# Kernel tuning notes

Hardware: AMD Instinct MI355X
Metric: run time of the kernel (lower is better)

The kernel has to match this reference:

```python
import jax, jax.numpy as jnp
import numpy as np
from jax import lax

DN = ('NCHW', 'OIHW', 'NCHW')

def conv2d(x, w, b, stride):
    y = lax.conv_general_dilated(x, w, (stride, stride), [(1, 1), (1, 1)], dimension_numbers=DN)
    return y + b[None, :, None, None]

def conv_transpose2d(x, w, b):
    # PyTorch ConvTranspose2d(k=3, stride=2, padding=1, output_padding=1)
    # == conv with lhs_dilation=2, pad low = k-1-p = 1, pad high = k-1-p+op = 2,
    # kernel spatially flipped and in/out channel dims swapped.  w: [in, out, kh, kw]
    wf = jnp.flip(w, (2, 3)).transpose(1, 0, 2, 3)  # [out, in, kh, kw]
    y = lax.conv_general_dilated(x, wf, (1, 1), [(1, 2), (1, 2)], lhs_dilation=(2, 2), dimension_numbers=DN)
    return y + b[None, :, None, None]

def setup_inputs() -> dict:
    key = jax.random.key(0)
    ks = jax.random.split(key, 20)
    s = 0.05
    inp = {
        'x':   jax.random.normal(ks[0], (64, 2, 256, 256), jnp.float32),
        'w1':  jax.random.normal(ks[1], (32, 2, 3, 3), jnp.float32) * s,
        'b1':  jnp.zeros((32,), jnp.float32),
        'w2':  jax.random.normal(ks[2], (64, 32, 3, 3), jnp.float32) * s,
        'b2':  jnp.zeros((64,), jnp.float32),
        'w3':  jax.random.normal(ks[3], (128, 64, 3, 3), jnp.float32) * s,
        'b3':  jnp.zeros((128,), jnp.float32),
        'w4':  jax.random.normal(ks[4], (128, 128, 3, 3), jnp.float32) * s,
        'b4':  jnp.zeros((128,), jnp.float32),
        'emb': jax.random.normal(ks[5], (512, 64), jnp.float32) * s,
        'dw1': jax.random.normal(ks[6], (128, 64, 3, 3), jnp.float32) * s,   # ConvTranspose2d weight [in, out, kh, kw]
        'db1': jnp.zeros((64,), jnp.float32),
        'dw2': jax.random.normal(ks[7], (64, 32, 3, 3), jnp.float32) * s,
        'db2': jnp.zeros((32,), jnp.float32),
        'dw3': jax.random.normal(ks[8], (32, 1, 3, 3), jnp.float32) * s,
        'db3': jnp.zeros((1,), jnp.float32),
    }
    return inp

def reference(x, w1, b1, w2, b2, w3, b3, w4, b4, emb, dw1, db1, dw2, db2, dw3, db3):
    # ---- Encoder ----
    h = jax.nn.relu(conv2d(x, w1, b1, 2))
    h = jax.nn.relu(conv2d(h, w2, b2, 2))
    h = jax.nn.relu(conv2d(h, w3, b3, 2))
    encoded = jax.nn.relu(conv2d(h, w4, b4, 1))  # [B, 128, H/8, W/8]

    # ---- VectorQuantizerEMA (inference math: cdist + argmin + lookup, straight-through) ----
    D = emb.shape[1]  # 64
    flat = encoded.reshape(encoded.shape[0], encoded.shape[1], -1).reshape(-1, D)  # [N, 64]
    dist = (jnp.sum(flat * flat, axis=1, keepdims=True)
            - 2.0 * flat @ emb.T
            + jnp.sum(emb * emb, axis=1)[None, :])  # [N, 512]
    idx = jnp.argmin(dist, axis=1)  # [N]
    quantized = emb[idx]            # [N, 64] gather
    q_st = flat + lax.stop_gradient(quantized - flat)  # straight-through estimator
    vq_feature = q_st.reshape(encoded.shape)

    # ---- Decoder ----
    d = jax.nn.relu(conv_transpose2d(vq_feature, dw1, db1))
    d = jax.nn.relu(conv_transpose2d(d, dw2, db2))
    decoded = conv_transpose2d(d, dw3, db3)  # [B, 1, 256, 256]
    return decoded
```

## Files before the change

kernel.cpp:

```cpp
#include <hip/hip_runtime.h>


using short8  = __attribute__((ext_vector_type(8))) short;
using short4v = __attribute__((ext_vector_type(4))) short;
using floatx4 = __attribute__((ext_vector_type(4))) float;

__device__ inline unsigned short bf16rn(float f) {
  unsigned u = __float_as_uint(f);
  unsigned r = (u + 0x7fffu + ((u >> 16) & 1u)) >> 16;
  return (unsigned short)r;
}
__device__ inline float bf2f1(short h) {
  return __uint_as_float(((unsigned)(unsigned short)h) << 16);
}

__device__ const int DKY[9]  = {1, 1, 1, 2, 0, 2, 2, 0, 0};
__device__ const int DKX[9]  = {1, 2, 0, 1, 1, 2, 0, 2, 0};

__global__ __launch_bounds__(256) void ring_zero(short* __restrict__ h,
                                                 short* __restrict__ l,
                                                 int nimg, int PH, int PW, int C) {
  const int RC = (2 * PW + 2 * (PH - 2)) * C;
  int t = blockIdx.x * 256 + threadIdx.x;
  if (t >= nimg * RC) return;
  const int nl = t / RC;
  int rem = t - nl * RC;
  const int p = rem / C;
  const int ch = rem - p * C;
  int r, c;
  if (p < 2 * PW) {
    r = (p < PW) ? 0 : PH - 1;
    c = (p < PW) ? p : p - PW;
  } else {
    int q = p - 2 * PW;
    if (q < PH - 2) { r = 1 + q; c = 0; }
    else { r = 1 + q - (PH - 2); c = PW - 1; }
  }
  const size_t a = (((size_t)nl * PH + r) * PW + c) * C + ch;
  h[a] = 0; l[a] = 0;
}

__global__ __launch_bounds__(256) void ring_zero1(short* __restrict__ h,
                                                  int nimg, int PH, int PW, int C) {
  const int RC = (2 * PW + 2 * (PH - 2)) * C;
  int t = blockIdx.x * 256 + threadIdx.x;
  if (t >= nimg * RC) return;
  const int nl = t / RC;
  int rem = t - nl * RC;
  const int p = rem / C;
  const int ch = rem - p * C;
  int r, c;
  if (p < 2 * PW) {
    r = (p < PW) ? 0 : PH - 1;
    c = (p < PW) ? p : p - PW;
  } else {
    int q = p - 2 * PW;
    if (q < PH - 2) { r = 1 + q; c = 0; }
    else { r = 1 + q - (PH - 2); c = PW - 1; }
  }
  h[(((size_t)nl * PH + r) * PW + c) * C + ch] = 0;
}

__global__ __launch_bounds__(256) void conv1_xt(const float* __restrict__ x,
                                                const float* __restrict__ w,
                                                const float* __restrict__ bias,
                                                short* __restrict__ oh,
                                                short* __restrict__ ol, int NH) {
  int t = blockIdx.x * 256 + threadIdx.x;
  if (t >= NH * 128 * 128) return;
  const int px = t & 16383;
  const int n  = t >> 14;
  const int r = px >> 7, c = px & 127;
  const int ih0 = 2 * r - 1, iw0 = 2 * c - 1;
  float acc[32];
#pragma unroll
  for (int o = 0; o < 32; ++o) acc[o] = bias[o];
  const float* ip = x + (size_t)n * 2 * 65536;
#pragma unroll
  for (int ic = 0; ic < 2; ++ic, ip += 65536) {
    float v[9];
#pragma unroll
    for (int kh = 0; kh < 3; ++kh) {
      const int ih = ih0 + kh;
#pragma unroll
      for (int kw = 0; kw < 3; ++kw) {
        const int iw = iw0 + kw;
        const bool ok = (ih >= 0) && (ih < 256) && (iw >= 0) && (iw < 256);
        v[kh * 3 + kw] = ok ? ip[ih * 256 + iw] : 0.f;
      }
    }
#pragma unroll
    for (int o = 0; o < 32; ++o) {
      float s = acc[o];
#pragma unroll
      for (int k = 0; k < 9; ++k) s = fmaf(v[k], w[(o * 2 + ic) * 9 + k], s);
      acc[o] = s;
    }
  }
  const size_t base = (((size_t)n * 130 + r + 1) * 130 + (c + 1)) * 32;
  short8 vh[4], vl[4];
#pragma unroll
  for (int g = 0; g < 4; ++g) {
#pragma unroll
    for (int kk = 0; kk < 8; ++kk) {
      const float rv = fmaxf(acc[g * 8 + kk], 0.f);
      const unsigned short hh = bf16rn(rv);
      vh[g][kk] = (short)hh;
      vl[g][kk] = (short)bf16rn(rv - __uint_as_float((unsigned)hh << 16));
    }
    *(short8*)(oh + base + g * 8) = vh[g];
    *(short8*)(ol + base + g * 8) = vl[g];
  }
}

template<int CIN, int COUT>
__global__ __launch_bounds__(256) void wprep_conv(const float* __restrict__ w,
                                                  short* __restrict__ hi,
                                                  short* __restrict__ lo) {
  constexpr int MT = COUT / 16;
  const int t = blockIdx.x * 256 + threadIdx.x;
  const int j = t & 7;
  const int lane = (t >> 3) & 63;
  const int g = t >> 9;
  const int mt = g % MT;
  const int s = g / MT;
  const int icb = s / 9, tap = s - icb * 9;
  const int kh = tap / 3, kw = tap - kh * 3;
  const int m = mt * 16 + (lane & 15);
  const int ic = icb * 32 + ((lane >> 4) << 3) + j;
  const float v = w[((m * CIN + ic) * 3 + kh) * 3 + kw];
  const unsigned short h = bf16rn(v);
  hi[t] = (short)h;
  lo[t] = (short)bf16rn(v - __uint_as_float((unsigned)h << 16));
}

template<int CIN, int COUT>
__global__ __launch_bounds__(256) void wprep_dec_h(const float* __restrict__ w,
                                                   short* __restrict__ hi) {
  constexpr int MT = COUT / 16, ICB = CIN / 32;
  const int t = blockIdx.x * 256 + threadIdx.x;
  const int j = t & 7;
  const int lane = (t >> 3) & 63;
  const int g = t >> 9;
  const int mt = g % MT;
  const int u = g / MT;
  const int icb = u % ICB;
  const int e = u / ICB;
  const int ky = DKY[e], kx = DKX[e];
  const int m = mt * 16 + (lane & 15);
  const int ic = icb * 32 + ((lane >> 4) << 3) + j;
  hi[t] = (short)bf16rn(w[((ic * COUT + m) * 3 + ky) * 3 + kx]);
}

template<int CIN, int COUT, int OH, int OW, int S, int PHI, int PWI, int PHO, int PWO, int NP>
__global__ __launch_bounds__(256) void conv_mfma_xt(
    const short* __restrict__ xih, const short* __restrict__ xil,
    const short* __restrict__ ah,  const short* __restrict__ al,
    const float* __restrict__ bias,
    short* __restrict__ xoh, short* __restrict__ xol) {
  constexpr int MT = COUT / 16, ICB = CIN / 32;
  constexpr int PXB = 64 * NP, TPB = OH * OW / PXB;
  const int b = blockIdx.x;
  const int n = b / TPB, pt = b % TPB;
  const int lane = threadIdx.x & 63, wave = threadIdx.x >> 6;
  const int quad = lane >> 4;
  int rr[NP], cc[NP];
  size_t bbase[NP];
#pragma unroll
  for (int p = 0; p < NP; ++p) {
    const int pl = pt * PXB + wave * (16 * NP) + p * 16 + (lane & 15);
    rr[p] = pl / OW; cc[p] = pl % OW;
    bbase[p] = (((size_t)n * PHI + S * rr[p]) * PWI + S * cc[p]) * CIN + quad * 8;
  }

  floatx4 acc[MT][NP];
#pragma unroll
  for (int mt = 0; mt < MT; ++mt)
#pragma unroll
    for (int p = 0; p < NP; ++p) acc[mt][p] = (floatx4){0.f, 0.f, 0.f, 0.f};

  const short8* __restrict__ ah8 = (const short8*)ah;
  const short8* __restrict__ al8 = (const short8*)al;

  for (int icb = 0; icb < ICB; ++icb) {
#pragma unroll
    for (int tap = 0; tap < 9; ++tap) {
      const int kh = tap / 3, kw = tap - kh * 3;
      short8 bh[NP], bl[NP];
#pragma unroll
      for (int p = 0; p < NP; ++p) {
        const size_t be = bbase[p] + (size_t)(kh * PWI + kw) * CIN + icb * 32;
        bh[p] = *(const short8*)(xih + be);
        bl[p] = *(const short8*)(xil + be);
      }
#pragma unroll
      for (int mt = 0; mt < MT; ++mt) {
        const int fi = ((icb * 9 + tap) * MT + mt) * 64 + lane;
        const short8 wh = ah8[fi];
        const short8 wl = al8[fi];
#pragma unroll
        for (int p = 0; p < NP; ++p) {
          acc[mt][p] = __builtin_amdgcn_mfma_f32_16x16x32_bf16(wh, bh[p], acc[mt][p], 0, 0, 0);
          acc[mt][p] = __builtin_amdgcn_mfma_f32_16x16x32_bf16(wh, bl[p], acc[mt][p], 0, 0, 0);
          acc[mt][p] = __builtin_amdgcn_mfma_f32_16x16x32_bf16(wl, bh[p], acc[mt][p], 0, 0, 0);
        }
      }
    }
  }
#pragma unroll
  for (int p = 0; p < NP; ++p) {
    const size_t ob = (((size_t)n * PHO + rr[p] + 1) * PWO + (cc[p] + 1)) * COUT + quad * 4;
#pragma unroll
    for (int mt = 0; mt < MT; ++mt) {
      short4v sh, sl;
#pragma unroll
      for (int q = 0; q < 4; ++q) {
        const float v = fmaxf(acc[mt][p][q] + bias[mt * 16 + quad * 4 + q], 0.f);
        const unsigned short hh = bf16rn(v);
        sh[q] = (short)hh;
        sl[q] = (short)bf16rn(v - __uint_as_float((unsigned)hh << 16));
      }
      *(short4v*)(xoh + ob + mt * 16) = sh;
      *(short4v*)(xol + ob + mt * 16) = sl;
    }
  }
}

template<int CIN, int COUT, int IH, int IW, int PHI, int PWI, int PHO, int PWO, int NP>
__global__ __launch_bounds__(256) void deconv_bf16_xt(
    const short* __restrict__ xih, const short* __restrict__ ah,
    const float* __restrict__ bias, short* __restrict__ xoh) {
  constexpr int MT = COUT / 16, ICB = CIN / 32;
  constexpr int PXB = 64 * NP, TPB = IH * IW / PXB;
  constexpr int PHE[9] = {0, 1, 1, 2, 2, 3, 3, 3, 3};
  constexpr int DE[9]  = {0, 0, 1, 0, 2, 0, 1, 2, 3};
  const int b = blockIdx.x;
  const int n = b / TPB, pt = b % TPB;
  const int lane = threadIdx.x & 63, wave = threadIdx.x >> 6;
  const int quad = lane >> 4;
  int ii[NP], jj[NP];
  size_t p00[NP];
#pragma unroll
  for (int p = 0; p < NP; ++p) {
    const int pl = pt * PXB + wave * (16 * NP) + p * 16 + (lane & 15);
    ii[p] = pl / IW; jj[p] = pl % IW;
    p00[p] = (((size_t)n * PHI + (ii[p] + 1)) * PWI + (jj[p] + 1)) * CIN + quad * 8;
  }

  floatx4 acc[4][MT][NP];
#pragma unroll
  for (int ph = 0; ph < 4; ++ph)
#pragma unroll
    for (int mt = 0; mt < MT; ++mt)
#pragma unroll
      for (int p = 0; p < NP; ++p) acc[ph][mt][p] = (floatx4){0.f, 0.f, 0.f, 0.f};

  const short8* __restrict__ ah8 = (const short8*)ah;
  for (int icb = 0; icb < ICB; ++icb) {
    short8 bh[NP][4];
#pragma unroll
    for (int p = 0; p < NP; ++p)
#pragma unroll
      for (int d = 0; d < 4; ++d)
        bh[p][d] = *(const short8*)(xih + p00[p] +
                                    (size_t)((d >> 1) * PWI + (d & 1)) * CIN + icb * 32);
#pragma unroll
    for (int e = 0; e < 9; ++e) {
      const int ph = PHE[e], d = DE[e];
#pragma unroll
      for (int mt = 0; mt < MT; ++mt) {
        const short8 wh = ah8[((e * ICB + icb) * MT + mt) * 64 + lane];
#pragma unroll
        for (int p = 0; p < NP; ++p)
          acc[ph][mt][p] = __builtin_amdgcn_mfma_f32_16x16x32_bf16(
              wh, bh[p][d], acc[ph][mt][p], 0, 0, 0);
      }
    }
  }
#pragma unroll
  for (int p = 0; p < NP; ++p)
#pragma unroll
    for (int ph = 0; ph < 4; ++ph) {
      const int oy = 2 * ii[p] + (ph >> 1), ox = 2 * jj[p] + (ph & 1);
      const size_t ob = (((size_t)n * PHO + oy + 1) * PWO + (ox + 1)) * COUT + quad * 4;
#pragma unroll
      for (int mt = 0; mt < MT; ++mt) {
        short4v sh;
#pragma unroll
        for (int q = 0; q < 4; ++q)
          sh[q] = (short)bf16rn(fmaxf(acc[ph][mt][p][q] + bias[mt * 16 + quad * 4 + q], 0.f));
        *(short4v*)(xoh + ob + mt * 16) = sh;
      }
    }
}

__global__ __launch_bounds__(256) void conv4_mfma(
    const short* __restrict__ xthi, const short* __restrict__ xtlo,
    const short* __restrict__ ahi,  const short* __restrict__ alo,
    const float* __restrict__ bias,
    short* __restrict__ ench, short* __restrict__ encl) {
  __shared__ short lh[6 * 34 * 32];
  __shared__ short ll[6 * 34 * 32];
  __shared__ short ash[2][4096];
  __shared__ short asl[2][4096];
  const int b    = blockIdx.x;
  const int n    = b >> 3;
  const int pt   = b & 7;
  const int r0   = pt * 4;
  const int tid  = threadIdx.x;
  const int lane = tid & 63;
  const int wave = tid >> 6;
  const int kq   = lane >> 4;
  int pl[2], lrow[2], lcol[2];
#pragma unroll
  for (int p = 0; p < 2; ++p) {
    pl[p] = pt * 128 + wave * 32 + p * 16 + (lane & 15);
    lrow[p] = (pl[p] >> 5) - r0;
    lcol[p] = pl[p] & 31;
  }

  floatx4 acc[8][2];
#pragma unroll
  for (int mt = 0; mt < 8; ++mt)
#pragma unroll
    for (int p = 0; p < 2; ++p) acc[mt][p] = (floatx4){0.f, 0.f, 0.f, 0.f};

  const short8* __restrict__ ah8 = (const short8*)ahi;
  const short8* __restrict__ al8 = (const short8*)alo;
  const short* __restrict__ ghbase = xthi + (((size_t)n * 34 + r0) * 34) * 128;
  const short* __restrict__ glbase = xtlo + (((size_t)n * 34 + r0) * 34) * 128;

  short8 rah0, rah1, ral0, ral1;
  rah0 = ah8[tid];        rah1 = ah8[tid + 256];
  ral0 = al8[tid];        ral1 = al8[tid + 256];
  *(short8*)(ash[0] + tid * 8) = rah0;
  *(short8*)(ash[0] + (tid + 256) * 8) = rah1;
  *(short8*)(asl[0] + tid * 8) = ral0;
  *(short8*)(asl[0] + (tid + 256) * 8) = ral1;

  int s = 0;
  for (int icb = 0; icb < 4; ++icb) {
    __syncthreads();
    {
      const short* gh = ghbase + icb * 32;
      const short* gl = glbase + icb * 32;
      for (int t = tid; t < 816; t += 256) {
        const int wr  = t * 8;
        const int row = wr / 1088;
        const int rem = wr - row * 1088;
        const int col = rem >> 5;
        const int ch  = rem & 31;
        const size_t g = ((size_t)(row * 34 + col)) * 128 + ch;
        *(short8*)(lh + wr) = *(const short8*)(gh + g);
        *(short8*)(ll + wr) = *(const short8*)(gl + g);
      }
    }
    __syncthreads();
#pragma unroll
    for (int tap = 0; tap < 9; ++tap, ++s) {
      if (s < 35) {
        const int nb = (s + 1) * 512;
        rah0 = ah8[nb + tid];        rah1 = ah8[nb + tid + 256];
        ral0 = al8[nb + tid];        ral1 = al8[nb + tid + 256];
      }
      const int kh = tap / 3, kw = tap - kh * 3;
      const short8* __restrict__ a8h = (const short8*)ash[s & 1];
      const short8* __restrict__ a8l = (const short8*)asl[s & 1];
      short8 bh[2], bl[2];
#pragma unroll
      for (int p = 0; p < 2; ++p) {
        const int le = ((lrow[p] + kh) * 34 + (lcol[p] + kw)) * 32 + kq * 8;
        bh[p] = *(const short8*)(lh + le);
        bl[p] = *(const short8*)(ll + le);
      }
#pragma unroll
      for (int mt = 0; mt < 8; ++mt) {
        const short8 ah = a8h[mt * 64 + lane];
        const short8 al = a8l[mt * 64 + lane];
#pragma unroll
        for (int p = 0; p < 2; ++p) {
          acc[mt][p] = __builtin_amdgcn_mfma_f32_16x16x32_bf16(ah, bh[p], acc[mt][p], 0, 0, 0);
          acc[mt][p] = __builtin_amdgcn_mfma_f32_16x16x32_bf16(ah, bl[p], acc[mt][p], 0, 0, 0);
          acc[mt][p] = __builtin_amdgcn_mfma_f32_16x16x32_bf16(al, bh[p], acc[mt][p], 0, 0, 0);
        }
      }
      if (s < 35) {
        const int nbuf = (s + 1) & 1;
        *(short8*)(ash[nbuf] + tid * 8) = rah0;
        *(short8*)(ash[nbuf] + (tid + 256) * 8) = rah1;
        *(short8*)(asl[nbuf] + tid * 8) = ral0;
        *(short8*)(asl[nbuf] + (tid + 256) * 8) = ral1;
        __syncthreads();
      }
    }
  }
#pragma unroll
  for (int p = 0; p < 2; ++p) {
    const size_t obase = (size_t)n * 128 * 1024 + pl[p];
#pragma unroll
    for (int mt = 0; mt < 8; ++mt) {
#pragma unroll
      for (int q = 0; q < 4; ++q) {
        const int cout = mt * 16 + kq * 4 + q;
        const float rr = fmaxf(acc[mt][p][q] + bias[cout], 0.f);
        const unsigned short h = bf16rn(rr);
        const size_t oi = obase + (size_t)cout * 1024;
        ench[oi] = (short)h;
        encl[oi] = (short)bf16rn(rr - __uint_as_float((unsigned)h << 16));
      }
    }
  }
}

__global__ __launch_bounds__(256) void vq_norms(const float* __restrict__ emb,
                                                float* __restrict__ norms) {
  int jj = blockIdx.x * 256 + threadIdx.x;
  if (jj < 512) {
    float s = 0.f;
    const float* e = emb + jj * 64;
#pragma unroll
    for (int k = 0; k < 64; ++k) s = fmaf(e[k], e[k], s);
    norms[jj] = s;
  }
}

__global__ __launch_bounds__(256) void emb_prep(const float* __restrict__ emb,
                                                short* __restrict__ hi,
                                                short* __restrict__ lo) {
  const int t = blockIdx.x * 256 + threadIdx.x;
  const int j  = t & 7;
  const int l  = (t >> 3) & 63;
  const int kk = (t >> 9) & 1;
  const int ct = t >> 10;
  const int code = ct * 16 + (l & 15);
  const int k = kk * 32 + ((l >> 4) << 3) + j;
  const float v = emb[code * 64 + k];
  const unsigned short h = bf16rn(v);
  hi[t] = (short)h;
  lo[t] = (short)bf16rn(v - __uint_as_float((unsigned)h << 16));
}

__global__ __launch_bounds__(256) void vq_mfma(
    const short* __restrict__ fhi, const short* __restrict__ flo,
    const short* __restrict__ ebh, const short* __restrict__ ebl,
    const float* __restrict__ nrm, const float* __restrict__ emb,
    short* __restrict__ d1h) {
  __shared__ int sidx[128];
  const int lane = threadIdx.x & 63;
  const int wave = threadIdx.x >> 6;
  const int n  = blockIdx.x >> 4;
  const int pb = blockIdx.x & 15;

  short8 ah0[2], ah1[2], al0[2], al1[2];
#pragma unroll
  for (int g = 0; g < 2; ++g) {
    const int ch = wave * 32 + g * 16 + (lane & 15);
    const size_t abase = (((size_t)(n * 128 + ch)) * 16 + pb) * 64 + ((lane >> 4) << 3);
    ah0[g] = *(const short8*)(fhi + abase);
    ah1[g] = *(const short8*)(fhi + abase + 32);
    al0[g] = *(const short8*)(flo + abase);
    al1[g] = *(const short8*)(flo + abase + 32);
  }

  float bestv[2][4];
  int   besti[2][4];
#pragma unroll
  for (int g = 0; g < 2; ++g)
#pragma unroll
    for (int q = 0; q < 4; ++q) { bestv[g][q] = 3.4e38f; besti[g][q] = 0; }

  const short8* __restrict__ ebh8 = (const short8*)ebh;
  const short8* __restrict__ ebl8 = (const short8*)ebl;
  for (int ct = 0; ct < 32; ++ct) {
    const int f0 = (ct * 2) * 64 + lane;
    const short8 b0h = ebh8[f0];
    const short8 b1h = ebh8[f0 + 64];
    const short8 b0l = ebl8[f0];
    const short8 b1l = ebl8[f0 + 64];
    const int code = ct * 16 + (lane & 15);
    const float nn = nrm[code];
#pragma unroll
    for (int g = 0; g < 2; ++g) {
      floatx4 acc = {0.f, 0.f, 0.f, 0.f};
      acc = __builtin_amdgcn_mfma_f32_16x16x32_bf16(ah0[g], b0h, acc, 0, 0, 0);
      acc = __builtin_amdgcn_mfma_f32_16x16x32_bf16(ah1[g], b1h, acc, 0, 0, 0);
      acc = __builtin_amdgcn_mfma_f32_16x16x32_bf16(ah0[g], b0l, acc, 0, 0, 0);
      acc = __builtin_amdgcn_mfma_f32_16x16x32_bf16(ah1[g], b1l, acc, 0, 0, 0);
      acc = __builtin_amdgcn_mfma_f32_16x16x32_bf16(al0[g], b0h, acc, 0, 0, 0);
      acc = __builtin_amdgcn_mfma_f32_16x16x32_bf16(al1[g], b1h, acc, 0, 0, 0);
#pragma unroll
      for (int q = 0; q < 4; ++q) {
        const float sc = nn - 2.f * acc[q];
        if (sc < bestv[g][q]) { bestv[g][q] = sc; besti[g][q] = code; }
      }
    }
  }
#pragma unroll
  for (int off = 1; off < 16; off <<= 1) {
#pragma unroll
    for (int g = 0; g < 2; ++g)
#pragma unroll
      for (int q = 0; q < 4; ++q) {
        const float ov = __shfl_xor(bestv[g][q], off, 64);
        const int   oi = __shfl_xor(besti[g][q], off, 64);
        if (ov < bestv[g][q] || (ov == bestv[g][q] && oi < besti[g][q])) {
          bestv[g][q] = ov; besti[g][q] = oi;
        }
      }
  }
  if ((lane & 15) == 0) {
#pragma unroll
    for (int g = 0; g < 2; ++g)
#pragma unroll
      for (int q = 0; q < 4; ++q)
        sidx[wave * 32 + g * 16 + (lane >> 4) * 4 + q] = besti[g][q];
  }
  __syncthreads();
  const int chg = (threadIdx.x & 15) * 8;
  int gi8[8];
#pragma unroll
  for (int k = 0; k < 8; ++k) gi8[k] = sidx[chg + k];
#pragma unroll
  for (int pxg = 0; pxg < 4; ++pxg) {
    const int p = pxg * 16 + (threadIdx.x >> 4);
    const int pix = pb * 64 + p;
    const int r = pix >> 5, c = pix & 31;
    short8 v;
#pragma unroll
    for (int k = 0; k < 8; ++k)
      v[k] = (short)bf16rn(emb[(size_t)gi8[k] * 64 + p]);
    *(short8*)(d1h + (((size_t)n * 34 + r + 1) * 34 + (c + 1)) * 128 + chg) = v;
  }
}

__global__ __launch_bounds__(256) void dec3_xt(const short* __restrict__ xh,
                                               const float* __restrict__ w,
                                               const float* __restrict__ bias,
                                               float* __restrict__ out, int NH) {
  int t = blockIdx.x * 256 + threadIdx.x;
  if (t >= NH * 128 * 128) return;
  const int px = t & 16383;
  const int nl = t >> 14;
  const int i = px >> 7, j = px & 127;
  const float b0 = bias[0];
  float a00 = b0, a01 = b0, a10 = b0, a11 = b0;
  const size_t base00 = (((size_t)nl * 130 + i + 1) * 130 + (j + 1)) * 32;
#pragma unroll
  for (int icg = 0; icg < 4; ++icg) {
    const short8 h00 = *(const short8*)(xh + base00 + icg * 8);
    const short8 h01 = *(const short8*)(xh + base00 + 32 + icg * 8);
    const short8 h10 = *(const short8*)(xh + base00 + 130 * 32 + icg * 8);
    const short8 h11 = *(const short8*)(xh + base00 + 130 * 32 + 32 + icg * 8);
#pragma unroll
    for (int kk = 0; kk < 8; ++kk) {
      const int ic = icg * 8 + kk;
      const float x00 = bf2f1(h00[kk]);
      const float x01 = bf2f1(h01[kk]);
      const float x10 = bf2f1(h10[kk]);
      const float x11 = bf2f1(h11[kk]);
      const float* wp = w + ic * 9;
      a00 = fmaf(x00, wp[4], a00);
      a01 = fmaf(x00, wp[5], fmaf(x01, wp[3], a01));
      a10 = fmaf(x00, wp[7], fmaf(x10, wp[1], a10));
      a11 = fmaf(x00, wp[8], fmaf(x01, wp[6], fmaf(x10, wp[2], fmaf(x11, wp[0], a11))));
    }
  }
  float* op = out + ((size_t)nl * 256 + 2 * i) * 256 + 2 * j;
  op[0] = a00; op[1] = a01; op[256] = a10; op[257] = a11;
}

extern "C" void kernel_launch(void* const* d_in, const int* in_sizes, int n_in,
                              void* d_out, int out_size, void* d_ws, size_t ws_size,
                              hipStream_t stream) {
  const float* x   = (const float*)d_in[0];
  const float* w1  = (const float*)d_in[1];
  const float* b1  = (const float*)d_in[2];
  const float* w2  = (const float*)d_in[3];
  const float* b2  = (const float*)d_in[4];
  const float* w3  = (const float*)d_in[5];
  const float* b3  = (const float*)d_in[6];
  const float* w4  = (const float*)d_in[7];
  const float* b4  = (const float*)d_in[8];
  const float* emb = (const float*)d_in[9];
  const float* dw1 = (const float*)d_in[10];
  const float* db1 = (const float*)d_in[11];
  const float* dw2 = (const float*)d_in[12];
  const float* db2 = (const float*)d_in[13];
  const float* dw3 = (const float*)d_in[14];
  const float* db3 = (const float*)d_in[15];
  float* outp = (float*)d_out;

  const int N = in_sizes[0] / (2 * 256 * 256);
  if (N & 1) return;
  const int NH = N / 2;

  const size_t sx3 = (size_t)N * 66 * 66 * 64;
  const size_t sx2 = (size_t)NH * 130 * 130 * 32;
  const size_t sx4 = (size_t)N * 34 * 34 * 128;
  const size_t se  = (size_t)N * 128 * 1024;
  const size_t sd1 = sx4;
  const size_t smalls = 512 + 18432 + 73728 + 147456 + 73728 + 18432 + 32768;
  const size_t need = (sx3 + sx4 + se + sd1 + smalls) * sizeof(float);
  if (ws_size < need) return;

  float* ws = (float*)d_ws;
  short* x3h = (short*)ws;                 short* x3l = x3h + sx3;
  short* x2h = (short*)(ws + sx3);         short* x2l = x2h + sx2;
  short* x4h = (short*)(ws + sx3);         short* x4l = x4h + sx4;
  short* ech = (short*)(ws + sx3 + sx4);   short* ecl = ech + se;
  short* d1h = (short*)(ws + sx3 + sx4 + se);
  short* d2h = (short*)ws;
  short* d3h = (short*)(ws + sx3);
  float* sm  = ws + sx3 + sx4 + se + sd1;
  float* nrm = sm;
  short* a2h = (short*)(sm + 512);                         short* a2l = a2h + 18432;
  short* a3h = (short*)(sm + 512 + 18432);                 short* a3l = a3h + 73728;
  short* a4h = (short*)(sm + 512 + 18432 + 73728);         short* a4l = a4h + 147456;
  short* ad1h = (short*)(sm + 512 + 18432 + 73728 + 147456);
  short* ad2h = (short*)(sm + 512 + 18432 + 73728 + 147456 + 73728);
  short* ebh = (short*)(sm + 512 + 18432 + 73728 + 147456 + 73728 + 18432); short* ebl = ebh + 32768;

  wprep_conv<32, 64><<<72, 256, 0, stream>>>(w2, a2h, a2l);
  wprep_conv<64, 128><<<288, 256, 0, stream>>>(w3, a3h, a3l);
  wprep_conv<128, 128><<<576, 256, 0, stream>>>(w4, a4h, a4l);
  wprep_dec_h<128, 64><<<288, 256, 0, stream>>>(dw1, ad1h);
  wprep_dec_h<64, 32><<<72, 256, 0, stream>>>(dw2, ad2h);
  vq_norms<<<2, 256, 0, stream>>>(emb, nrm);
  emb_prep<<<128, 256, 0, stream>>>(emb, ebh, ebl);

  ring_zero<<<(int)((NH * 516 * 32 + 255) / 256), 256, 0, stream>>>(x2h, x2l, NH, 130, 130, 32);
  ring_zero<<<(int)(((size_t)N * 260 * 64 + 255) / 256), 256, 0, stream>>>(x3h, x3l, N, 66, 66, 64);
  for (int half = 0; half < 2; ++half) {
    const int n0 = half * NH;
    conv1_xt<<<NH * 16384 / 256, 256, 0, stream>>>(
        x + (size_t)n0 * 2 * 65536, w1, b1, x2h, x2l, NH);
    conv_mfma_xt<32, 64, 64, 64, 2, 130, 130, 66, 66, 2>
        <<<NH * 32, 256, 0, stream>>>(x2h, x2l, a2h, a2l, b2,
                                      x3h + (size_t)n0 * 66 * 66 * 64,
                                      x3l + (size_t)n0 * 66 * 66 * 64);
  }
  ring_zero<<<(int)(((size_t)N * 132 * 128 + 255) / 256), 256, 0, stream>>>(x4h, x4l, N, 34, 34, 128);
  conv_mfma_xt<64, 128, 32, 32, 2, 66, 66, 34, 34, 2>
      <<<N * 8, 256, 0, stream>>>(x3h, x3l, a3h, a3l, b3, x4h, x4l);
  conv4_mfma<<<N * 8, 256, 0, stream>>>(x4h, x4l, a4h, a4l, b4, ech, ecl);

  ring_zero1<<<(int)(((size_t)N * 132 * 128 + 255) / 256), 256, 0, stream>>>(d1h, N, 34, 34, 128);
  vq_mfma<<<N * 16, 256, 0, stream>>>(ech, ecl, ebh, ebl, nrm, emb, d1h);

  ring_zero1<<<(int)(((size_t)N * 260 * 64 + 255) / 256), 256, 0, stream>>>(d2h, N, 66, 66, 64);
  deconv_bf16_xt<128, 64, 32, 32, 34, 34, 66, 66, 2>
      <<<N * 8, 256, 0, stream>>>(d1h, ad1h, db1, d2h);
  ring_zero1<<<(int)((NH * 516 * 32 + 255) / 256), 256, 0, stream>>>(d3h, NH, 130, 130, 32);
  for (int half = 0; half < 2; ++half) {
    const int n0 = half * NH;
    deconv_bf16_xt<64, 32, 64, 64, 66, 66, 130, 130, 2>
        <<<NH * 32, 256, 0, stream>>>(d2h + (size_t)n0 * 66 * 66 * 64,
                                      ad2h, db2, d3h);
    dec3_xt<<<NH * 16384 / 256, 256, 0, stream>>>(
        d3h, dw3, db3, outp + (size_t)n0 * 65536, NH);
  }
}
```

Baseline: 655.8 us.

## Stage conv/deconv weights in double-buffered LDS and merge prep kernels

The conv_mfma_xt kernel now stages each tap's weight fragments through double-buffered shared memory, prefetching the next slice into registers while MFMAs run. The first deconv does the same for a whole input-channel block of weights. The seven small weight and embedding prep kernels are merged into one launch. The aim is to cut redundant per-wave global weight loads and launch overhead, at the cost of a __syncthreads per tap and extra LDS traffic.

```diff
diff --git a/kernel.cpp b/kernel.cpp
--- a/kernel.cpp
+++ b/kernel.cpp
@@ -114,11 +114,10 @@
 }
 
 template<int CIN, int COUT>
-__global__ __launch_bounds__(256) void wprep_conv(const float* __restrict__ w,
-                                                  short* __restrict__ hi,
-                                                  short* __restrict__ lo) {
+__device__ inline void wprep_conv_body(int t, const float* __restrict__ w,
+                                       short* __restrict__ hi,
+                                       short* __restrict__ lo) {
   constexpr int MT = COUT / 16;
-  const int t = blockIdx.x * 256 + threadIdx.x;
   const int j = t & 7;
   const int lane = (t >> 3) & 63;
   const int g = t >> 9;
@@ -135,10 +134,9 @@
 }
 
 template<int CIN, int COUT>
-__global__ __launch_bounds__(256) void wprep_dec_h(const float* __restrict__ w,
-                                                   short* __restrict__ hi) {
+__device__ inline void wprep_dec_body(int t, const float* __restrict__ w,
+                                      short* __restrict__ hi) {
   constexpr int MT = COUT / 16, ICB = CIN / 32;
-  const int t = blockIdx.x * 256 + threadIdx.x;
   const int j = t & 7;
   const int lane = (t >> 3) & 63;
   const int g = t >> 9;
@@ -152,6 +150,52 @@
   hi[t] = (short)bf16rn(w[((ic * COUT + m) * 3 + ky) * 3 + kx]);
 }
 
+__global__ __launch_bounds__(256) void prep_all(
+    const float* __restrict__ w2, const float* __restrict__ w3,
+    const float* __restrict__ w4, const float* __restrict__ dw1,
+    const float* __restrict__ dw2, const float* __restrict__ emb,
+    short* __restrict__ a2h, short* __restrict__ a2l,
+    short* __restrict__ a3h, short* __restrict__ a3l,
+    short* __restrict__ a4h, short* __restrict__ a4l,
+    short* __restrict__ ad1h, short* __restrict__ ad2h,
+    float* __restrict__ nrm, short* __restrict__ ebh,
+    short* __restrict__ ebl) {
+  const int bb = blockIdx.x;
+  const int tid = threadIdx.x;
+  if (bb < 72) {
+    wprep_conv_body<32, 64>(bb * 256 + tid, w2, a2h, a2l);
+  } else if (bb < 360) {
+    wprep_conv_body<64, 128>((bb - 72) * 256 + tid, w3, a3h, a3l);
+  } else if (bb < 936) {
+    wprep_conv_body<128, 128>((bb - 360) * 256 + tid, w4, a4h, a4l);
+  } else if (bb < 1224) {
+    wprep_dec_body<128, 64>((bb - 936) * 256 + tid, dw1, ad1h);
+  } else if (bb < 1296) {
+    wprep_dec_body<64, 32>((bb - 1224) * 256 + tid, dw2, ad2h);
+  } else if (bb < 1424) {
+    const int t = (bb - 1296) * 256 + tid;
+    const int j  = t & 7;
+    const int l  = (t >> 3) & 63;
+    const int kk = (t >> 9) & 1;
+    const int ct = t >> 10;
+    const int code = ct * 16 + (l & 15);
+    const int k = kk * 32 + ((l >> 4) << 3) + j;
+    const float v = emb[code * 64 + k];
+    const unsigned short h = bf16rn(v);
+    ebh[t] = (short)h;
+    ebl[t] = (short)bf16rn(v - __uint_as_float((unsigned)h << 16));
+  } else {
+    const int jj = (bb - 1424) * 256 + tid;
+    if (jj < 512) {
+      float s = 0.f;
+      const float* e = emb + jj * 64;
+#pragma unroll
+      for (int k = 0; k < 64; ++k) s = fmaf(e[k], e[k], s);
+      nrm[jj] = s;
+    }
+  }
+}
+
 template<int CIN, int COUT, int OH, int OW, int S, int PHI, int PWI, int PHO, int PWO, int NP>
 __global__ __launch_bounds__(256) void conv_mfma_xt(
     const short* __restrict__ xih, const short* __restrict__ xil,
@@ -160,9 +204,15 @@
     short* __restrict__ xoh, short* __restrict__ xol) {
   constexpr int MT = COUT / 16, ICB = CIN / 32;
   constexpr int PXB = 64 * NP, TPB = OH * OW / PXB;
+  constexpr int NSL = ICB * 9;
+  constexpr int CH  = MT * 64;
+  constexpr int CPT = (CH + 255) / 256;
+  __shared__ short ash[2][CH * 8];
+  __shared__ short asl2[2][CH * 8];
   const int b = blockIdx.x;
   const int n = b / TPB, pt = b % TPB;
-  const int lane = threadIdx.x & 63, wave = threadIdx.x >> 6;
+  const int tid = threadIdx.x;
+  const int lane = tid & 63, wave = tid >> 6;
   const int quad = lane >> 4;
   int rr[NP], cc[NP];
   size_t bbase[NP];
@@ -182,9 +232,34 @@
   const short8* __restrict__ ah8 = (const short8*)ah;
   const short8* __restrict__ al8 = (const short8*)al;
 
+  short8 ra[CPT], rl[CPT];
+#pragma unroll
+  for (int c = 0; c < CPT; ++c) {
+    const int idx = tid + c * 256;
+    if (idx < CH) { ra[c] = ah8[idx]; rl[c] = al8[idx]; }
+  }
+#pragma unroll
+  for (int c = 0; c < CPT; ++c) {
+    const int idx = tid + c * 256;
+    if (idx < CH) {
+      *(short8*)(ash[0] + idx * 8) = ra[c];
+      *(short8*)(asl2[0] + idx * 8) = rl[c];
+    }
+  }
+  __syncthreads();
+
+  int s = 0;
   for (int icb = 0; icb < ICB; ++icb) {
 #pragma unroll
-    for (int tap = 0; tap < 9; ++tap) {
+    for (int tap = 0; tap < 9; ++tap, ++s) {
+      if (s + 1 < NSL) {
+        const int base = (s + 1) * CH;
+#pragma unroll
+        for (int c = 0; c < CPT; ++c) {
+          const int idx = tid + c * 256;
+          if (idx < CH) { ra[c] = ah8[base + idx]; rl[c] = al8[base + idx]; }
+        }
+      }
       const int kh = tap / 3, kw = tap - kh * 3;
       short8 bh[NP], bl[NP];
 #pragma unroll
@@ -193,11 +268,12 @@
         bh[p] = *(const short8*)(xih + be);
         bl[p] = *(const short8*)(xil + be);
       }
+      const short8* __restrict__ a8h = (const short8*)ash[s & 1];
+      const short8* __restrict__ a8l = (const short8*)asl2[s & 1];
 #pragma unroll
       for (int mt = 0; mt < MT; ++mt) {
-        const int fi = ((icb * 9 + tap) * MT + mt) * 64 + lane;
-        const short8 wh = ah8[fi];
-        const short8 wl = al8[fi];
+        const short8 wh = a8h[mt * 64 + lane];
+        const short8 wl = a8l[mt * 64 + lane];
 #pragma unroll
         for (int p = 0; p < NP; ++p) {
           acc[mt][p] = __builtin_amdgcn_mfma_f32_16x16x32_bf16(wh, bh[p], acc[mt][p], 0, 0, 0);
@@ -205,6 +281,18 @@
           acc[mt][p] = __builtin_amdgcn_mfma_f32_16x16x32_bf16(wl, bh[p], acc[mt][p], 0, 0, 0);
         }
       }
+      if (s + 1 < NSL) {
+        const int nb = (s + 1) & 1;
+#pragma unroll
+        for (int c = 0; c < CPT; ++c) {
+          const int idx = tid + c * 256;
+          if (idx < CH) {
+            *(short8*)(ash[nb] + idx * 8) = ra[c];
+            *(short8*)(asl2[nb] + idx * 8) = rl[c];
+          }
+        }
+        __syncthreads();
+      }
     }
   }
 #pragma unroll
@@ -226,17 +314,21 @@
   }
 }
 
-template<int CIN, int COUT, int IH, int IW, int PHI, int PWI, int PHO, int PWO, int NP>
+template<int CIN, int COUT, int IH, int IW, int PHI, int PWI, int PHO, int PWO, int NP, int ASTG>
 __global__ __launch_bounds__(256) void deconv_bf16_xt(
     const short* __restrict__ xih, const short* __restrict__ ah,
     const float* __restrict__ bias, short* __restrict__ xoh) {
   constexpr int MT = COUT / 16, ICB = CIN / 32;
   constexpr int PXB = 64 * NP, TPB = IH * IW / PXB;
+  constexpr int CHI = 9 * MT * 64;
+  constexpr int CPT = (CHI + 255) / 256;
   constexpr int PHE[9] = {0, 1, 1, 2, 2, 3, 3, 3, 3};
   constexpr int DE[9]  = {0, 0, 1, 0, 2, 0, 1, 2, 3};
+  __shared__ short ash[ASTG ? 2 * CHI * 8 : 1];
   const int b = blockIdx.x;
   const int n = b / TPB, pt = b % TPB;
-  const int lane = threadIdx.x & 63, wave = threadIdx.x >> 6;
+  const int tid = threadIdx.x;
+  const int lane = tid & 63, wave = tid >> 6;
   const int quad = lane >> 4;
   int ii[NP], jj[NP];
   size_t p00[NP];
@@ -256,6 +348,26 @@
       for (int p = 0; p < NP; ++p) acc[ph][mt][p] = (floatx4){0.f, 0.f, 0.f, 0.f};
 
   const short8* __restrict__ ah8 = (const short8*)ah;
+
+  short8 ra[ASTG ? CPT : 1];
+  if constexpr (ASTG) {
+#pragma unroll
+    for (int c = 0; c < CPT; ++c) {
+      const int idx = tid + c * 256;
+      if (idx < CHI) {
+        const int e = idx / (MT * 64);
+        const int rem = idx - e * (MT * 64);
+        ra[c] = ah8[(e * ICB + 0) * (MT * 64) + rem];
+      }
+    }
+#pragma unroll
+    for (int c = 0; c < CPT; ++c) {
+      const int idx = tid + c * 256;
+      if (idx < CHI) *(short8*)(ash + idx * 8) = ra[c];
+    }
+    __syncthreads();
+  }
+
   for (int icb = 0; icb < ICB; ++icb) {
     short8 bh[NP][4];
 #pragma unroll
@@ -264,16 +376,44 @@
       for (int d = 0; d < 4; ++d)
         bh[p][d] = *(const short8*)(xih + p00[p] +
                                     (size_t)((d >> 1) * PWI + (d & 1)) * CIN + icb * 32);
+    if constexpr (ASTG) {
+      if (icb + 1 < ICB) {
+#pragma unroll
+        for (int c = 0; c < CPT; ++c) {
+          const int idx = tid + c * 256;
+          if (idx < CHI) {
+            const int e = idx / (MT * 64);
+            const int rem = idx - e * (MT * 64);
+            ra[c] = ah8[(e * ICB + icb + 1) * (MT * 64) + rem];
+          }
+        }
+      }
+    }
 #pragma unroll
     for (int e = 0; e < 9; ++e) {
       const int ph = PHE[e], d = DE[e];
 #pragma unroll
       for (int mt = 0; mt < MT; ++mt) {
-        const short8 wh = ah8[((e * ICB + icb) * MT + mt) * 64 + lane];
+        short8 wh;
+        if constexpr (ASTG)
+          wh = ((const short8*)(ash + (size_t)(icb & 1) * CHI * 8))[(e * MT + mt) * 64 + lane];
+        else
+          wh = ah8[((e * ICB + icb) * MT + mt) * 64 + lane];
 #pragma unroll
         for (int p = 0; p < NP; ++p)
           acc[ph][mt][p] = __builtin_amdgcn_mfma_f32_16x16x32_bf16(
               wh, bh[p][d], acc[ph][mt][p], 0, 0, 0);
+      }
+    }
+    if constexpr (ASTG) {
+      if (icb + 1 < ICB) {
+        const size_t nb = (size_t)((icb + 1) & 1) * CHI * 8;
+#pragma unroll
+        for (int c = 0; c < CPT; ++c) {
+          const int idx = tid + c * 256;
+          if (idx < CHI) *(short8*)(ash + nb + idx * 8) = ra[c];
+        }
+        __syncthreads();
       }
     }
   }
@@ -410,34 +550,6 @@
       }
     }
   }
-}
-
-__global__ __launch_bounds__(256) void vq_norms(const float* __restrict__ emb,
-                                                float* __restrict__ norms) {
-  int jj = blockIdx.x * 256 + threadIdx.x;
-  if (jj < 512) {
-    float s = 0.f;
-    const float* e = emb + jj * 64;
-#pragma unroll
-    for (int k = 0; k < 64; ++k) s = fmaf(e[k], e[k], s);
-    norms[jj] = s;
-  }
-}
-
-__global__ __launch_bounds__(256) void emb_prep(const float* __restrict__ emb,
-                                                short* __restrict__ hi,
-                                                short* __restrict__ lo) {
-  const int t = blockIdx.x * 256 + threadIdx.x;
-  const int j  = t & 7;
-  const int l  = (t >> 3) & 63;
-  const int kk = (t >> 9) & 1;
-  const int ct = t >> 10;
-  const int code = ct * 16 + (l & 15);
-  const int k = kk * 32 + ((l >> 4) << 3) + j;
-  const float v = emb[code * 64 + k];
-  const unsigned short h = bf16rn(v);
-  hi[t] = (short)h;
-  lo[t] = (short)bf16rn(v - __uint_as_float((unsigned)h << 16));
 }
 
 __global__ __launch_bounds__(256) void vq_mfma(
@@ -620,13 +732,9 @@
   short* ad2h = (short*)(sm + 512 + 18432 + 73728 + 147456 + 73728);
   short* ebh = (short*)(sm + 512 + 18432 + 73728 + 147456 + 73728 + 18432); short* ebl = ebh + 32768;
 
-  wprep_conv<32, 64><<<72, 256, 0, stream>>>(w2, a2h, a2l);
-  wprep_conv<64, 128><<<288, 256, 0, stream>>>(w3, a3h, a3l);
-  wprep_conv<128, 128><<<576, 256, 0, stream>>>(w4, a4h, a4l);
-  wprep_dec_h<128, 64><<<288, 256, 0, stream>>>(dw1, ad1h);
-  wprep_dec_h<64, 32><<<72, 256, 0, stream>>>(dw2, ad2h);
-  vq_norms<<<2, 256, 0, stream>>>(emb, nrm);
-  emb_prep<<<128, 256, 0, stream>>>(emb, ebh, ebl);
+  prep_all<<<1426, 256, 0, stream>>>(w2, w3, w4, dw1, dw2, emb,
+                                     a2h, a2l, a3h, a3l, a4h, a4l,
+                                     ad1h, ad2h, nrm, ebh, ebl);
 
   ring_zero<<<(int)((NH * 516 * 32 + 255) / 256), 256, 0, stream>>>(x2h, x2l, NH, 130, 130, 32);
   ring_zero<<<(int)(((size_t)N * 260 * 64 + 255) / 256), 256, 0, stream>>>(x3h, x3l, N, 66, 66, 64);
@@ -648,12 +756,12 @@
   vq_mfma<<<N * 16, 256, 0, stream>>>(ech, ecl, ebh, ebl, nrm, emb, d1h);
 
   ring_zero1<<<(int)(((size_t)N * 260 * 64 + 255) / 256), 256, 0, stream>>>(d2h, N, 66, 66, 64);
-  deconv_bf16_xt<128, 64, 32, 32, 34, 34, 66, 66, 2>
+  deconv_bf16_xt<128, 64, 32, 32, 34, 34, 66, 66, 2, 1>
       <<<N * 8, 256, 0, stream>>>(d1h, ad1h, db1, d2h);
   ring_zero1<<<(int)((NH * 516 * 32 + 255) / 256), 256, 0, stream>>>(d3h, NH, 130, 130, 32);
   for (int half = 0; half < 2; ++half) {
     const int n0 = half * NH;
-    deconv_bf16_xt<64, 32, 64, 64, 66, 66, 130, 130, 2>
+    deconv_bf16_xt<64, 32, 64, 64, 66, 66, 130, 130, 2, 0>
         <<<NH * 32, 256, 0, stream>>>(d2h + (size_t)n0 * 66 * 66 * 64,
                                       ad2h, db2, d3h);
     dec3_xt<<<NH * 16384 / 256, 256, 0, stream>>>(
```

Result: faster. 629.1 us (-4.1%).
